# Kernel optimization log

Hardware: AMD Instinct MI355X
Metric: run time of the kernel (lower is better)

## Reference

```python
import jax, jax.numpy as jnp
import numpy as np

N = 4096      # vertices (ring graph)
R = 3         # ring connectivity radius -> n = 2R+1 = 7 neighbors (incl. self)
C0, C1, C2 = 16, 32, 32


def _build_graph():
    v = np.arange(N)

    def rfield(l):
        off = np.arange(-l * R, l * R + 1)
        return np.sort((v[:, None] + off[None, :]) % N, axis=1)  # [N, 2lR+1]

    rf0, rf1, rf2 = rfield(0), rfield(1), rfield(2)
    nbrs = rf1  # neighborhood(v, 1), sorted, includes v

    def chi_idx(rf_v, rf_prev):
        # position of each element of v's rfield inside each neighbor's prev rfield
        rfp = rf_prev[nbrs]                                   # [N, n, Kp]
        eq = rf_v[:, None, :, None] == rfp[:, :, None, :]     # [N, n, K, Kp]
        mask = eq.any(-1).astype(np.float32)                  # element present?
        idx = eq.argmax(-1).astype(np.int32)                  # gather index (0 if absent)
        return idx, mask

    idx1, mask1 = chi_idx(rf1, rf0)
    idx2, mask2 = chi_idx(rf2, rf1)

    def sub_adj(rf):
        d = np.abs(rf[:, :, None] - rf[:, None, :])
        d = np.minimum(d, N - d)
        return ((d >= 1) & (d <= R)).astype(np.float32)       # [N, K, K]

    return nbrs.astype(np.int32), idx1, mask1, idx2, mask2, sub_adj(rf1), sub_adj(rf2)


def setup_inputs() -> dict:
    key = jax.random.key(0)
    ks = jax.random.split(key, 10)
    nbrs, idx1, mask1, idx2, mask2, adj1, adj2 = _build_graph()
    return {
        "labels": jax.random.normal(ks[0], (N, C0), jnp.float32),
        "nbrs": jnp.asarray(nbrs),
        "idx1": jnp.asarray(idx1), "mask1": jnp.asarray(mask1),
        "idx2": jnp.asarray(idx2), "mask2": jnp.asarray(mask2),
        "adj1": jnp.asarray(adj1), "adj2": jnp.asarray(adj2),
        "W1": jax.random.normal(ks[1], (C1, C0), jnp.float32) * 0.1,
        "b1": jax.random.normal(ks[2], (C1,), jnp.float32) * 0.1,
        "W2": jax.random.normal(ks[3], (C2, C1), jnp.float32) * 0.1,
        "b2": jax.random.normal(ks[4], (C2,), jnp.float32) * 0.1,
        "al1": jax.random.normal(ks[5], (1,), jnp.float32),
        "al2": jax.random.normal(ks[6], (1,), jnp.float32),
        "Wfc": jax.random.normal(ks[7], (1, C2), jnp.float32) * 0.1,
        "bfc": jax.random.normal(ks[8], (1,), jnp.float32) * 0.1,
    }


def _level(feat_prev, nbrs, idx, mask, adj, al, W, b):
    # feat_prev: [N, C, Kp, Kp]; idx/mask: [N, n, K]; adj: [N, K, K]
    g = feat_prev[nbrs]                                          # [N, n, C, Kp, Kp]
    g = jnp.take_along_axis(g, idx[:, :, None, :, None], axis=3)  # [N, n, C, K, Kp]
    g = jnp.take_along_axis(g, idx[:, :, None, None, :], axis=4)  # [N, n, C, K, K]
    g = g * mask[:, :, None, :, None] * mask[:, :, None, None, :]  # chi F chi^T
    agg = g.sum(axis=1) + al * adj[:, None, :, :]                # [N, C, K, K]
    n_, C, K, _ = agg.shape
    x = agg.reshape(n_, K * K, C)            # faithful to torch .view(k*k, -1)
    y = jax.nn.relu(x @ W.T + b)             # [N, K*K, Cout]
    return y.reshape(n_, W.shape[0], K, K)   # faithful to torch .view(out, k, k)


def reference(labels, nbrs, idx1, mask1, idx2, mask2, adj1, adj2,
              W1, b1, W2, b2, al1, al2, Wfc, bfc):
    feat0 = labels.reshape(N, C0, 1, 1)
    f1 = _level(feat0, nbrs, idx1, mask1, adj1, al1, W1, b1)
    f2 = _level(f1, nbrs, idx2, mask2, adj2, al2, W2, b2)
    g_repr = f2.sum(axis=(2, 3)).sum(axis=0, keepdims=True)      # [1, C2]
    output = g_repr @ Wfc.T + bfc                                # [1, 1]
    return output, g_repr
```

## Files before the change

kernel.cpp:

```cpp
#include <hip/hip_runtime.h>

#define NV 4096
#define NMASK 4095
#define NN 7
#define KK1 49
#define KK2 169
#define C0 16
#define C1 32
#define C2 32
#define F1LEN 1568
#define RSTR 882
#define QSTR 18
#define VB 4
#define NB (NV / VB)
#define NT 704
#define WROWS 10
#define LROWS 16
#define TIL 31

typedef unsigned int uint;
typedef unsigned short ushort;
typedef __attribute__((ext_vector_type(8))) short short8v;
typedef __attribute__((ext_vector_type(4))) float float4v;

static __device__ __forceinline__ ushort f2bf(float f) {
    union { float f; uint u; } v; v.f = f;
    uint r = (v.u + 0x7fffu + ((v.u >> 16) & 1u)) >> 16;
    return (ushort)r;
}
static __device__ __forceinline__ float bflo(uint w) { return __uint_as_float(w << 16); }
static __device__ __forceinline__ float bfhi(uint w) { return __uint_as_float(w & 0xffff0000u); }

__global__ __launch_bounds__(704) void fused_kernel(
    const float* __restrict__ labels, const int* __restrict__ nbrs,
    const float* __restrict__ mask1, const int* __restrict__ idx2,
    const float* __restrict__ mask2, const float* __restrict__ adj1,
    const float* __restrict__ adj2, const float* __restrict__ W1,
    const float* __restrict__ b1, const float* __restrict__ W2,
    const float* __restrict__ b2, const float* __restrict__ al1,
    const float* __restrict__ al2, float* __restrict__ gpart)
{
    __shared__ __align__(16) uint   fs[WROWS * RSTR];
    __shared__ __align__(16) ushort aggT[VB * 5408];
    __shared__ int   rowOf2[VB][NN];
    __shared__ float grs[32];
    __shared__ float al1s, al2s;

    float* aggf = (float*)aggT;
    float* Lw   = (float*)((char*)aggT + 31360);
    float* m1w  = (float*)((char*)aggT + 32384);
    int*   nbrW = (int*)  ((char*)aggT + 34344);

    int t = threadIdx.x;
    int v0 = blockIdx.x * VB;
    int lane = t & 63, wvid = t >> 6;
    int r16 = lane & 15, kg = lane >> 4;

    if (t < 32) grs[t] = 0.f;
    if (t == 0) { al1s = al1[0]; al2s = al2[0]; }
    for (int e = t; e < LROWS * 16; e += NT)
        Lw[e] = labels[(size_t)(((v0 - 6 + (e >> 4)) + NV) & NMASK) * 16 + (e & 15)];
    for (int e = t; e < WROWS * 49; e += NT)
        m1w[e] = mask1[(size_t)(((v0 - 3 + e / 49) + NV) & NMASK) * 49 + (e % 49)];
    for (int e = t; e < WROWS * NN; e += NT) {
        int r = e / NN, u = e % NN;
        nbrW[e] = (nbrs[(size_t)(((v0 - 3 + r) + NV) & NMASK) * NN + u] - v0 + 6 + NV) & NMASK;
    }
    for (int e = t; e < VB * NN; e += NT)
        rowOf2[e / NN][e % NN] = (nbrs[v0 * NN + e] - v0 + 3 + NV) & NMASK;
    __syncthreads();

    if (t < WROWS * 49) {
        int r = t / 49, ij = t % 49, i = ij / 7, j = ij % 7;
        float a[16];
        #pragma unroll
        for (int c = 0; c < 16; ++c) a[c] = 0.f;
        #pragma unroll
        for (int u = 0; u < NN; ++u) {
            float mm = m1w[r * 49 + u * 7 + i] * m1w[r * 49 + u * 7 + j];
            const float4* lr = (const float4*)&Lw[nbrW[r * 7 + u] * 16];
            float4 l0 = lr[0], l1 = lr[1], l2 = lr[2], l3 = lr[3];
            a[0]+=mm*l0.x; a[1]+=mm*l0.y; a[2]+=mm*l0.z; a[3]+=mm*l0.w;
            a[4]+=mm*l1.x; a[5]+=mm*l1.y; a[6]+=mm*l1.z; a[7]+=mm*l1.w;
            a[8]+=mm*l2.x; a[9]+=mm*l2.y; a[10]+=mm*l2.z; a[11]+=mm*l2.w;
            a[12]+=mm*l3.x; a[13]+=mm*l3.y; a[14]+=mm*l3.z; a[15]+=mm*l3.w;
        }
        float av = al1s * adj1[(size_t)(((v0 - 3 + r) + NV) & NMASK) * 49 + ij];
        #pragma unroll
        for (int c = 0; c < 16; ++c)
            aggf[r * 784 + c * 49 + ij] = a[c] + av;
    }
    __syncthreads();

    {
        short8v wb0, wb1;
        #pragma unroll
        for (int e = 0; e < 8; ++e) {
            int k = kg * 8 + e;
            wb0[e] = (k < 16) ? (short)f2bf(W1[r16 * 16 + k]) : (short)0;
            wb1[e] = (k < 16) ? (short)f2bf(W1[(r16 + 16) * 16 + k]) : (short)0;
        }
        float bb0 = b1[r16], bb1 = b1[r16 + 16];
        ushort* fsh = (ushort*)fs;
        for (int tile = wvid; tile < TIL; tile += 11) {
            int m = tile * 16 + r16;
            short8v a;
            #pragma unroll
            for (int e = 0; e < 8; ++e) a[e] = 0;
            if (kg < 2 && m < WROWS * 49) {
                int r = m / 49, p = m % 49;
                const float4* xp = (const float4*)(aggf + r * 784 + p * 16 + kg * 8);
                float4 xa = xp[0], xb = xp[1];
                a[0]=(short)f2bf(xa.x); a[1]=(short)f2bf(xa.y); a[2]=(short)f2bf(xa.z); a[3]=(short)f2bf(xa.w);
                a[4]=(short)f2bf(xb.x); a[5]=(short)f2bf(xb.y); a[6]=(short)f2bf(xb.z); a[7]=(short)f2bf(xb.w);
            }
            float4v z = {0.f, 0.f, 0.f, 0.f};
            float4v d0 = __builtin_amdgcn_mfma_f32_16x16x32_bf16(a, wb0, z, 0, 0, 0);
            float4v d1 = __builtin_amdgcn_mfma_f32_16x16x32_bf16(a, wb1, z, 0, 0, 0);
            #pragma unroll
            for (int rr = 0; rr < 4; ++rr) {
                int m2 = tile * 16 + kg * 4 + rr;
                if (m2 < WROWS * 49) {
                    int r = m2 / 49, p = m2 % 49;
                    int f2a = p * 32 + r16;
                    int ca = f2a / 49, qa = f2a % 49;
                    int wa = (ca >> 1) ^ ((qa >> 4) << 1);
                    fsh[(r * RSTR + qa * QSTR + wa) * 2 + (ca & 1)] = f2bf(fmaxf(d0[rr] + bb0, 0.f));
                    int f2b = f2a + 16;
                    int cb = f2b / 49, qb = f2b % 49;
                    int wb = (cb >> 1) ^ ((qb >> 4) << 1);
                    fsh[(r * RSTR + qb * QSTR + wb) * 2 + (cb & 1)] = f2bf(fmaxf(d1[rr] + bb1, 0.f));
                }
            }
        }
    }
    __syncthreads();

    if (t < VB * KK2) {
        int vl = t / KK2, ij = t % KK2, i = ij / 13, j = ij % 13;
        int v = v0 + vl;
        const float* mb = mask2 + (size_t)v * 91;
        const int*   ib = idx2 + (size_t)v * 91;
        float acc[32];
        #pragma unroll
        for (int c = 0; c < 32; ++c) acc[c] = 0.f;
        #pragma unroll
        for (int u = 0; u < NN; ++u) {
            float mm = mb[u * 13 + i] * mb[u * 13 + j];
            int q = ib[u * 13 + i] * 7 + ib[u * 13 + j];
            const uint* base = fs + rowOf2[vl][u] * RSTR + q * QSTR;
            int sw = (q >> 4) << 1;
            #pragma unroll
            for (int e = 0; e < 8; ++e) {
                uint2 d = *(const uint2*)(base + ((2 * e) ^ sw));
                acc[4*e+0] += mm * bflo(d.x);
                acc[4*e+1] += mm * bfhi(d.x);
                acc[4*e+2] += mm * bflo(d.y);
                acc[4*e+3] += mm * bfhi(d.y);
            }
        }
        float av = al2s * adj2[(size_t)v * KK2 + ij];
        #pragma unroll
        for (int c = 0; c < 32; ++c)
            aggT[vl * 5408 + c * KK2 + ij] = f2bf(acc[c] + av);
    }
    __syncthreads();

    {
        short8v cb0, cb1;
        #pragma unroll
        for (int e = 0; e < 8; ++e) {
            cb0[e] = (short)f2bf(W2[r16 * 32 + kg * 8 + e]);
            cb1[e] = (short)f2bf(W2[(r16 + 16) * 32 + kg * 8 + e]);
        }
        float bias0 = b2[r16], bias1 = b2[r16 + 16];
        int p0 = wvid * 16;
        int prow = p0 + r16; if (prow > 168) prow = 168;
        float s0[4] = {0.f,0.f,0.f,0.f}, s1[4] = {0.f,0.f,0.f,0.f};
        #pragma unroll
        for (int vl = 0; vl < VB; ++vl) {
            const uint4* ap = (const uint4*)((const char*)aggT + vl * 10816 + prow * 64 + kg * 16);
            uint4 araw = *ap;
            short8v a = *reinterpret_cast<short8v*>(&araw);
            float4v z = {0.f, 0.f, 0.f, 0.f};
            float4v d0 = __builtin_amdgcn_mfma_f32_16x16x32_bf16(a, cb0, z, 0, 0, 0);
            float4v d1 = __builtin_amdgcn_mfma_f32_16x16x32_bf16(a, cb1, z, 0, 0, 0);
            #pragma unroll
            for (int r = 0; r < 4; ++r) {
                s0[r] += fmaxf(d0[r] + bias0, 0.f);
                s1[r] += fmaxf(d1[r] + bias1, 0.f);
            }
        }
        int chA = (p0 * 32) / KK2;
        float part0 = 0.f, part1 = 0.f, part2 = 0.f, part3 = 0.f;
        #pragma unroll
        for (int r = 0; r < 4; ++r) {
            int p = p0 + kg * 4 + r;
            if (p < KK2) {
                int c0 = (p * 32 + r16) / KK2 - chA;
                part0 += (c0 == 0) ? s0[r] : 0.f;
                part1 += (c0 == 1) ? s0[r] : 0.f;
                part2 += (c0 == 2) ? s0[r] : 0.f;
                part3 += (c0 == 3) ? s0[r] : 0.f;
                int c1 = (p * 32 + r16 + 16) / KK2 - chA;
                part0 += (c1 == 0) ? s1[r] : 0.f;
                part1 += (c1 == 1) ? s1[r] : 0.f;
                part2 += (c1 == 2) ? s1[r] : 0.f;
                part3 += (c1 == 3) ? s1[r] : 0.f;
            }
        }
        #pragma unroll
        for (int off = 32; off > 0; off >>= 1) {
            part0 += __shfl_xor(part0, off);
            part1 += __shfl_xor(part1, off);
            part2 += __shfl_xor(part2, off);
            part3 += __shfl_xor(part3, off);
        }
        if (lane == 0) {
            atomicAdd(&grs[chA], part0);
            if (chA + 1 < 32) atomicAdd(&grs[chA + 1], part1);
            if (chA + 2 < 32) atomicAdd(&grs[chA + 2], part2);
            if (chA + 3 < 32) atomicAdd(&grs[chA + 3], part3);
        }
    }
    __syncthreads();
    if (t < 32) gpart[blockIdx.x * 32 + t] = grs[t];
}

__global__ __launch_bounds__(1024) void fc_kernel(
    const float* __restrict__ gpart, const float* __restrict__ Wfc,
    const float* __restrict__ bfc, float* __restrict__ out)
{
    __shared__ float red[32][33];
    int t = threadIdx.x;
    int ch = t & 31, seg = t >> 5;
    float s = 0.f;
    for (int b = seg; b < NB; b += 32) s += gpart[b * 32 + ch];
    red[seg][ch] = s;
    __syncthreads();
    if (t < 32) {
        float g = 0.f;
        #pragma unroll
        for (int k = 0; k < 32; ++k) g += red[k][t];
        out[1 + t] = g;
        red[0][t] = g * Wfc[t];
    }
    __syncthreads();
    if (t == 0) {
        float p = bfc[0];
        #pragma unroll
        for (int k = 0; k < 32; ++k) p += red[0][k];
        out[0] = p;
    }
}

__global__ __launch_bounds__(64) void lvl1_kernel(
    const float* __restrict__ labels, const int* __restrict__ nbrs,
    const float* __restrict__ mask1, const float* __restrict__ adj1,
    const float* __restrict__ W1, const float* __restrict__ b1,
    const float* __restrict__ al1, float* __restrict__ f1out)
{
    __shared__ float Ls[NN][C0];
    __shared__ float m1s[NN][7];
    __shared__ float a1s[KK1];
    __shared__ float aggsh[C0 * KK1];
    __shared__ float W1s[C1 * 17];
    __shared__ float b1s[C1];
    int v = blockIdx.x, t = threadIdx.x;
    for (int e = t; e < NN * C0; e += 64) {
        int u = e >> 4, c = e & 15;
        Ls[u][c] = labels[(size_t)nbrs[v * NN + u] * C0 + c];
    }
    for (int e = t; e < KK1; e += 64) {
        m1s[e / 7][e % 7] = mask1[(size_t)v * KK1 + e];
        a1s[e] = adj1[(size_t)v * KK1 + e];
    }
    for (int e = t; e < C1 * C0; e += 64) W1s[(e >> 4) * 17 + (e & 15)] = W1[e];
    if (t < C1) b1s[t] = b1[t];
    float alpha = al1[0];
    __syncthreads();
    for (int e = t; e < C0 * KK1; e += 64) {
        int c = e / KK1, ij = e % KK1, i = ij / 7, j = ij % 7;
        float s = 0.f;
        #pragma unroll
        for (int u = 0; u < NN; ++u) s += Ls[u][c] * (m1s[u][i] * m1s[u][j]);
        aggsh[e] = s + alpha * a1s[ij];
    }
    __syncthreads();
    int co = t & 31;
    for (int e = t; e < F1LEN; e += 64) {
        int p = e >> 5;
        float s = b1s[co];
        #pragma unroll
        for (int c = 0; c < C0; ++c) s += aggsh[p * C0 + c] * W1s[co * 17 + c];
        f1out[(size_t)v * F1LEN + e] = fmaxf(s, 0.f);
    }
}

#define F1PAD 56
#define AGPAD 177
__global__ __launch_bounds__(192) void lvl2_kernel(
    const float* __restrict__ f1, const int* __restrict__ nbrs,
    const int* __restrict__ idx2, const float* __restrict__ mask2,
    const float* __restrict__ adj2, const float* __restrict__ W2,
    const float* __restrict__ b2, const float* __restrict__ al2,
    float* __restrict__ gr)
{
    __shared__ float f1s[C1 * F1PAD];
    __shared__ float aggT2[C1 * AGPAD];
    __shared__ float W2s[C2 * C1];
    __shared__ float b2s[C2];
    __shared__ float grs[C2];
    __shared__ int nbs[NN];
    int v = blockIdx.x, t = threadIdx.x;
    if (t < NN) nbs[t] = nbrs[v * NN + t];
    if (t < C2) { b2s[t] = b2[t]; grs[t] = 0.f; }
    for (int e = t; e < C2 * C1; e += 192) W2s[e] = W2[e];
    float alpha = al2[0];
    bool act = (t < KK2);
    float mmr[NN]; int qr[NN];
    float acc[C1];
    if (act) {
        int i = t / 13, j = t % 13;
        const float* mbase = mask2 + (size_t)v * NN * 13;
        const int* ibase = idx2 + (size_t)v * NN * 13;
        #pragma unroll
        for (int u = 0; u < NN; ++u) {
            mmr[u] = mbase[u * 13 + i] * mbase[u * 13 + j];
            qr[u] = ibase[u * 13 + i] * 7 + ibase[u * 13 + j];
        }
    }
    #pragma unroll
    for (int c = 0; c < C1; ++c) acc[c] = 0.f;
    int dst[9]; int nd = 0;
    for (int e = t; e < F1LEN; e += 192) dst[nd++] = (e / 49) * F1PAD + (e % 49);
    for (int u = 0; u < NN; ++u) {
        __syncthreads();
        const float* src = f1 + (size_t)nbs[u] * F1LEN;
        { int k = 0; for (int e = t; e < F1LEN; e += 192) f1s[dst[k++]] = src[e]; }
        __syncthreads();
        if (act) {
            float mv = mmr[u]; int q = qr[u];
            #pragma unroll
            for (int c = 0; c < C1; ++c) acc[c] += mv * f1s[c * F1PAD + q];
        }
    }
    if (act) {
        float a2v = alpha * adj2[(size_t)v * KK2 + t];
        #pragma unroll
        for (int c = 0; c < C1; ++c) {
            int f = c * KK2 + t;
            aggT2[(f & 31) * AGPAD + (f >> 5)] = acc[c] + a2v;
        }
    }
    __syncthreads();
    if (act) {
        int p = t;
        float ar[C1];
        #pragma unroll
        for (int c2 = 0; c2 < C1; ++c2) ar[c2] = aggT2[c2 * AGPAD + p];
        int chA = (p * 32) / KK2;
        int csplit = KK2 - (p * 32 - chA * KK2);
        float sA = 0.f, sB = 0.f;
        #pragma unroll
        for (int co = 0; co < C2; ++co) {
            float s = b2s[co];
            #pragma unroll
            for (int k = 0; k < 8; ++k) {
                float4 wv = *(const float4*)(&W2s[co * C1 + 4 * k]);
                s += ar[4*k+0]*wv.x + ar[4*k+1]*wv.y + ar[4*k+2]*wv.z + ar[4*k+3]*wv.w;
            }
            s = fmaxf(s, 0.f);
            if (co < csplit) sA += s; else sB += s;
        }
        atomicAdd(&grs[chA], sA);
        if (csplit < 32) atomicAdd(&grs[chA + 1], sB);
    }
    __syncthreads();
    if (t < C2) atomicAdd(&gr[t], grs[t]);
}

__global__ __launch_bounds__(64) void fc_small_kernel(
    const float* __restrict__ gr, const float* __restrict__ Wfc,
    const float* __restrict__ bfc, float* __restrict__ out)
{
    int t = threadIdx.x;
    float g = (t < C2) ? gr[t] : 0.f;
    if (t < C2) out[1 + t] = g;
    float p = (t < C2) ? g * Wfc[t] : 0.f;
    #pragma unroll
    for (int off = 32; off > 0; off >>= 1) p += __shfl_down(p, off);
    if (t == 0) out[0] = p + bfc[0];
}

extern "C" void kernel_launch(void* const* d_in, const int* in_sizes, int n_in,
                              void* d_out, int out_size, void* d_ws, size_t ws_size,
                              hipStream_t stream)
{
    const float* labels = (const float*)d_in[0];
    const int*   nbrs   = (const int*)d_in[1];
    const float* mask1  = (const float*)d_in[3];
    const int*   idx2   = (const int*)d_in[4];
    const float* mask2  = (const float*)d_in[5];
    const float* adj1   = (const float*)d_in[6];
    const float* adj2   = (const float*)d_in[7];
    const float* W1     = (const float*)d_in[8];
    const float* b1     = (const float*)d_in[9];
    const float* W2     = (const float*)d_in[10];
    const float* b2     = (const float*)d_in[11];
    const float* al1    = (const float*)d_in[12];
    const float* al2    = (const float*)d_in[13];
    const float* Wfc    = (const float*)d_in[14];
    const float* bfc    = (const float*)d_in[15];

    if (ws_size >= (size_t)NB * 32 * sizeof(float) + 128) {
        float* gpart = (float*)d_ws;
        fused_kernel<<<NB, NT, 0, stream>>>(labels, nbrs, mask1, idx2, mask2,
                                            adj1, adj2, W1, b1, W2, b2, al1, al2, gpart);
        fc_kernel<<<1, 1024, 0, stream>>>(gpart, Wfc, bfc, (float*)d_out);
    } else {
        float* f1 = (float*)d_ws;
        float* gr = (float*)((char*)d_ws + (size_t)NV * F1LEN * sizeof(float));
        hipMemsetAsync(gr, 0, C2 * sizeof(float), stream);
        lvl1_kernel<<<NV, 64, 0, stream>>>(labels, nbrs, mask1, adj1, W1, b1, al1, f1);
        lvl2_kernel<<<NV, 192, 0, stream>>>(f1, nbrs, idx2, mask2, adj2, W2, b2, al2, gr);
        fc_small_kernel<<<1, 64, 0, stream>>>(gr, Wfc, bfc, (float*)d_out);
    }
}
```

Before: 58.02 us.

## Fold final FC reduction into fused kernel via last-block ticket; stage mask2/idx2 in LDS

Removes the separate fc_kernel launch by having each block take an atomic ticket, with the last block to finish reducing all partial sums and writing the output. It adds a memset of the counter before the launch. Level-2 mask and index data are staged into shared memory as float/uchar and preloaded into registers instead of being read repeatedly from global memory. It also adds a min-blocks hint of 6 to launch_bounds. Risks are added register pressure, a serialized tail in the last block, and the extra memset launch.

```diff
diff --git a/kernel.cpp b/kernel.cpp
--- a/kernel.cpp
+++ b/kernel.cpp
@@ -20,6 +20,7 @@
 
 typedef unsigned int uint;
 typedef unsigned short ushort;
+typedef unsigned char uchar;
 typedef __attribute__((ext_vector_type(8))) short short8v;
 typedef __attribute__((ext_vector_type(4))) float float4v;
 
@@ -31,20 +32,25 @@
 static __device__ __forceinline__ float bflo(uint w) { return __uint_as_float(w << 16); }
 static __device__ __forceinline__ float bfhi(uint w) { return __uint_as_float(w & 0xffff0000u); }
 
-__global__ __launch_bounds__(704) void fused_kernel(
+__global__ __launch_bounds__(704, 6) void fused_kernel(
     const float* __restrict__ labels, const int* __restrict__ nbrs,
     const float* __restrict__ mask1, const int* __restrict__ idx2,
     const float* __restrict__ mask2, const float* __restrict__ adj1,
     const float* __restrict__ adj2, const float* __restrict__ W1,
     const float* __restrict__ b1, const float* __restrict__ W2,
     const float* __restrict__ b2, const float* __restrict__ al1,
-    const float* __restrict__ al2, float* __restrict__ gpart)
+    const float* __restrict__ al2, const float* __restrict__ Wfc,
+    const float* __restrict__ bfc, float* __restrict__ gpart,
+    uint* __restrict__ cnt, float* __restrict__ out)
 {
     __shared__ __align__(16) uint   fs[WROWS * RSTR];
     __shared__ __align__(16) ushort aggT[VB * 5408];
+    __shared__ float m2s[VB][91];
+    __shared__ uchar i2q[VB][96];
     __shared__ int   rowOf2[VB][NN];
     __shared__ float grs[32];
     __shared__ float al1s, al2s;
+    __shared__ uint  ticket;
 
     float* aggf = (float*)aggT;
     float* Lw   = (float*)((char*)aggT + 31360);
@@ -65,6 +71,11 @@
     for (int e = t; e < WROWS * NN; e += NT) {
         int r = e / NN, u = e % NN;
         nbrW[e] = (nbrs[(size_t)(((v0 - 3 + r) + NV) & NMASK) * NN + u] - v0 + 6 + NV) & NMASK;
+    }
+    for (int e = t; e < VB * 91; e += NT) {
+        int vl = e / 91, x = e % 91;
+        m2s[vl][x] = mask2[(size_t)v0 * 91 + e];
+        i2q[vl][x] = (uchar)idx2[(size_t)v0 * 91 + e];
     }
     for (int e = t; e < VB * NN; e += NT)
         rowOf2[e / NN][e % NN] = (nbrs[v0 * NN + e] - v0 + 3 + NV) & NMASK;
@@ -138,17 +149,21 @@
 
     if (t < VB * KK2) {
         int vl = t / KK2, ij = t % KK2, i = ij / 13, j = ij % 13;
-        int v = v0 + vl;
-        const float* mb = mask2 + (size_t)v * 91;
-        const int*   ib = idx2 + (size_t)v * 91;
+        float mmr[NN]; int qr[NN]; int rwr[NN];
+        #pragma unroll
+        for (int u = 0; u < NN; ++u) {
+            mmr[u] = m2s[vl][u * 13 + i] * m2s[vl][u * 13 + j];
+            qr[u]  = (int)i2q[vl][u * 13 + i] * 7 + (int)i2q[vl][u * 13 + j];
+            rwr[u] = rowOf2[vl][u];
+        }
         float acc[32];
         #pragma unroll
         for (int c = 0; c < 32; ++c) acc[c] = 0.f;
         #pragma unroll
         for (int u = 0; u < NN; ++u) {
-            float mm = mb[u * 13 + i] * mb[u * 13 + j];
-            int q = ib[u * 13 + i] * 7 + ib[u * 13 + j];
-            const uint* base = fs + rowOf2[vl][u] * RSTR + q * QSTR;
+            float mm = mmr[u];
+            int q = qr[u];
+            const uint* base = fs + rwr[u] * RSTR + q * QSTR;
             int sw = (q >> 4) << 1;
             #pragma unroll
             for (int e = 0; e < 8; ++e) {
@@ -159,7 +174,7 @@
                 acc[4*e+3] += mm * bfhi(d.y);
             }
         }
-        float av = al2s * adj2[(size_t)v * KK2 + ij];
+        float av = al2s * adj2[(size_t)(v0 + vl) * KK2 + ij];
         #pragma unroll
         for (int c = 0; c < 32; ++c)
             aggT[vl * 5408 + c * KK2 + ij] = f2bf(acc[c] + av);
@@ -225,32 +240,32 @@
     }
     __syncthreads();
     if (t < 32) gpart[blockIdx.x * 32 + t] = grs[t];
-}
-
-__global__ __launch_bounds__(1024) void fc_kernel(
-    const float* __restrict__ gpart, const float* __restrict__ Wfc,
-    const float* __restrict__ bfc, float* __restrict__ out)
-{
-    __shared__ float red[32][33];
-    int t = threadIdx.x;
-    int ch = t & 31, seg = t >> 5;
-    float s = 0.f;
-    for (int b = seg; b < NB; b += 32) s += gpart[b * 32 + ch];
-    red[seg][ch] = s;
-    __syncthreads();
-    if (t < 32) {
-        float g = 0.f;
-        #pragma unroll
-        for (int k = 0; k < 32; ++k) g += red[k][t];
-        out[1 + t] = g;
-        red[0][t] = g * Wfc[t];
-    }
-    __syncthreads();
-    if (t == 0) {
-        float p = bfc[0];
-        #pragma unroll
-        for (int k = 0; k < 32; ++k) p += red[0][k];
-        out[0] = p;
+
+    __threadfence();
+    if (t == 0) ticket = atomicAdd(cnt, 1);
+    __syncthreads();
+    if (ticket == NB - 1) {
+        __threadfence();
+        float* red = (float*)aggT;
+        int ch = t & 31, seg = t >> 5;
+        float s = 0.f;
+        for (int b = seg; b < NB; b += 22) s += gpart[b * 32 + ch];
+        red[seg * 32 + ch] = s;
+        __syncthreads();
+        if (t < 32) {
+            float g = 0.f;
+            #pragma unroll
+            for (int k = 0; k < 22; ++k) g += red[k * 32 + t];
+            out[1 + t] = g;
+            red[704 + t] = g * Wfc[t];
+        }
+        __syncthreads();
+        if (t == 0) {
+            float p = bfc[0];
+            #pragma unroll
+            for (int k = 0; k < 32; ++k) p += red[704 + k];
+            out[0] = p;
+        }
     }
 }
 
@@ -413,11 +428,15 @@
     const float* Wfc    = (const float*)d_in[14];
     const float* bfc    = (const float*)d_in[15];
 
-    if (ws_size >= (size_t)NB * 32 * sizeof(float) + 128) {
+    const size_t gpart_bytes = (size_t)NB * 32 * sizeof(float);
+
+    if (ws_size >= gpart_bytes + 64) {
         float* gpart = (float*)d_ws;
+        uint*  cnt   = (uint*)((char*)d_ws + gpart_bytes);
+        hipMemsetAsync(cnt, 0, sizeof(uint), stream);
         fused_kernel<<<NB, NT, 0, stream>>>(labels, nbrs, mask1, idx2, mask2,
-                                            adj1, adj2, W1, b1, W2, b2, al1, al2, gpart);
-        fc_kernel<<<1, 1024, 0, stream>>>(gpart, Wfc, bfc, (float*)d_out);
+                                            adj1, adj2, W1, b1, W2, b2, al1, al2,
+                                            Wfc, bfc, gpart, cnt, (float*)d_out);
     } else {
         float* f1 = (float*)d_ws;
         float* gr = (float*)((char*)d_ws + (size_t)NV * F1LEN * sizeof(float));
```

New measurement: 214.7 us. 270% more time.
